# Kernel tuning notes

Hardware: AMD Instinct MI355X
Metric: run time of the kernel (lower is better)

The kernel has to match this reference:

```python
import jax, jax.numpy as jnp
import numpy as np

VOCAB = 100000
EMBED = 128
B = 65536
K = 10
EPS = 1e-10


def setup_inputs() -> dict:
    key = jax.random.key(0)
    k1, k2, k3, k4, k5 = jax.random.split(key, 5)
    init = 0.5 / EMBED
    t_weight = jax.random.uniform(k1, (VOCAB, EMBED), jnp.float32, -init, init)
    c_weight = jax.random.uniform(k2, (VOCAB, EMBED), jnp.float32, -init, init)
    t = jax.random.randint(k3, (B,), 0, VOCAB)
    c = jax.random.randint(k4, (B,), 0, VOCAB)
    n = jax.random.randint(k5, (B, K), 0, VOCAB)
    return {"t_weight": t_weight, "c_weight": c_weight, "t": t, "c": c, "n": n}


def reference(t_weight, c_weight, t, c, n):
    vt = t_weight[t]          # [B, D]
    vc = c_weight[c]          # [B, D]
    vn = c_weight[n]          # [B, K, D]
    pos_score = jnp.sum(vt * vc, axis=1)                     # [B]
    pos_loss = -jnp.mean(jnp.log(jax.nn.sigmoid(pos_score) + EPS))
    neg_score = jnp.einsum('bkd,bd->bk', vn, vt)             # [B, K]
    neg_loss = -jnp.mean(jnp.sum(jnp.log(jax.nn.sigmoid(-neg_score) + EPS), axis=1))
    return pos_loss + neg_loss
```

## Files before the change

kernel.cpp:

```cpp
#include <hip/hip_runtime.h>
#include <hip/hip_bf16.h>

constexpr int kEmbed = 128;
constexpr int kBatch = 65536;
constexpr int kNeg   = 10;
constexpr float kEps = 1e-10f;

__global__ __launch_bounds__(256, 4) void sgns_loss_kernel(
    const float* __restrict__ tw,
    const float* __restrict__ cw,
    const int*   __restrict__ t,
    const int*   __restrict__ c,
    const int*   __restrict__ n,
    float*       __restrict__ out)
{
    const int tid     = threadIdx.x;
    const int lane    = tid & 31;
    const int group   = (blockIdx.x * blockDim.x + tid) >> 5;
    const int ngroups = (gridDim.x * blockDim.x) >> 5;

    float acc = 0.0f;

    for (int b = group; b < kBatch; b += ngroups) {
        const int it = t[b];
        const int ic = c[b];
        int ni[kNeg];
        #pragma unroll
        for (int k = 0; k < kNeg; ++k) ni[k] = n[b * kNeg + k];

        const float4 vt = *reinterpret_cast<const float4*>(tw + (size_t)it * kEmbed + 4 * lane);
        const float4 vc = *reinterpret_cast<const float4*>(cw + (size_t)ic * kEmbed + 4 * lane);

        float s[kNeg + 1];
        s[0] = vt.x * vc.x + vt.y * vc.y + vt.z * vc.z + vt.w * vc.w;

        #pragma unroll
        for (int k = 0; k < kNeg; ++k) {
            const float4 vn = *reinterpret_cast<const float4*>(
                cw + (size_t)ni[k] * kEmbed + 4 * lane);
            s[k + 1] = vt.x * vn.x + vt.y * vn.y + vt.z * vn.z + vt.w * vn.w;
        }

        #pragma unroll
        for (int k = 0; k < kNeg + 1; ++k) {
            float v = s[k];
            v += __shfl_xor(v, 16);
            v += __shfl_xor(v, 8);
            v += __shfl_xor(v, 4);
            v += __shfl_xor(v, 2);
            v += __shfl_xor(v, 1);
            s[k] = v;
        }

        float lb = __logf(1.0f / (1.0f + __expf(-s[0])) + kEps);
        #pragma unroll
        for (int k = 1; k < kNeg + 1; ++k)
            lb += __logf(1.0f / (1.0f + __expf(s[k])) + kEps);

        if (lane == 0) acc += lb;
    }

    #pragma unroll
    for (int m = 32; m >= 1; m >>= 1) acc += __shfl_xor(acc, m);

    __shared__ float wave_sum[4];
    if ((tid & 63) == 0) wave_sum[tid >> 6] = acc;
    __syncthreads();
    if (tid == 0) {
        const float s4 = wave_sum[0] + wave_sum[1] + wave_sum[2] + wave_sum[3];
        atomicAdd(out, s4 * (-1.0f / (float)kBatch));
    }
}

extern "C" void kernel_launch(void* const* d_in, const int* in_sizes, int n_in,
                              void* d_out, int out_size, void* d_ws, size_t ws_size,
                              hipStream_t stream) {
    const float* tw = (const float*)d_in[0];
    const float* cw = (const float*)d_in[1];
    const int*   t  = (const int*)d_in[2];
    const int*   c  = (const int*)d_in[3];
    const int*   n  = (const int*)d_in[4];
    float* out = (float*)d_out;

    hipMemsetAsync(out, 0, sizeof(float), stream);

    sgns_loss_kernel<<<2048, 256, 0, stream>>>(tw, cw, t, c, n, out);
}
```

Measured before the change: 162.7 us.

## Map each sample to 8 threads with 64-byte loads, drop grid-stride loop

Each batch row is now handled by 8 lanes, each loading four float4 values (64 bytes) per embedding row, instead of 32 lanes each loading one float4. This cuts the shuffle reduction from five steps to three and puts more rows in flight per wave. The grid-stride loop is removed, so the fixed grid of 2048 blocks of 256 threads covers exactly 65536 rows. The cost is higher register pressure and a hard dependence on that launch geometry.

```diff
diff --git a/kernel.cpp b/kernel.cpp
--- a/kernel.cpp
+++ b/kernel.cpp
@@ -14,52 +14,56 @@
     const int*   __restrict__ n,
     float*       __restrict__ out)
 {
-    const int tid     = threadIdx.x;
-    const int lane    = tid & 31;
-    const int group   = (blockIdx.x * blockDim.x + tid) >> 5;
-    const int ngroups = (gridDim.x * blockDim.x) >> 5;
+    const int tid = threadIdx.x;
+    const int b   = (blockIdx.x * blockDim.x + tid) >> 3;
+    const int sub = tid & 7;
+    const int col = sub * 16;
 
-    float acc = 0.0f;
+    const int it = t[b];
+    const int ic = c[b];
+    int ni[kNeg];
+    #pragma unroll
+    for (int k = 0; k < kNeg; ++k) ni[k] = n[b * kNeg + k];
 
-    for (int b = group; b < kBatch; b += ngroups) {
-        const int it = t[b];
-        const int ic = c[b];
-        int ni[kNeg];
-        #pragma unroll
-        for (int k = 0; k < kNeg; ++k) ni[k] = n[b * kNeg + k];
+    const float4* vtp = reinterpret_cast<const float4*>(tw + (size_t)it * kEmbed + col);
+    const float4 vt0 = vtp[0], vt1 = vtp[1], vt2 = vtp[2], vt3 = vtp[3];
 
-        const float4 vt = *reinterpret_cast<const float4*>(tw + (size_t)it * kEmbed + 4 * lane);
-        const float4 vc = *reinterpret_cast<const float4*>(cw + (size_t)ic * kEmbed + 4 * lane);
+    float s[kNeg + 1];
 
-        float s[kNeg + 1];
-        s[0] = vt.x * vc.x + vt.y * vc.y + vt.z * vc.z + vt.w * vc.w;
-
-        #pragma unroll
-        for (int k = 0; k < kNeg; ++k) {
-            const float4 vn = *reinterpret_cast<const float4*>(
-                cw + (size_t)ni[k] * kEmbed + 4 * lane);
-            s[k + 1] = vt.x * vn.x + vt.y * vn.y + vt.z * vn.z + vt.w * vn.w;
-        }
-
-        #pragma unroll
-        for (int k = 0; k < kNeg + 1; ++k) {
-            float v = s[k];
-            v += __shfl_xor(v, 16);
-            v += __shfl_xor(v, 8);
-            v += __shfl_xor(v, 4);
-            v += __shfl_xor(v, 2);
-            v += __shfl_xor(v, 1);
-            s[k] = v;
-        }
-
-        float lb = __logf(1.0f / (1.0f + __expf(-s[0])) + kEps);
-        #pragma unroll
-        for (int k = 1; k < kNeg + 1; ++k)
-            lb += __logf(1.0f / (1.0f + __expf(s[k])) + kEps);
-
-        if (lane == 0) acc += lb;
+    {
+        const float4* vcp = reinterpret_cast<const float4*>(cw + (size_t)ic * kEmbed + col);
+        const float4 a = vcp[0], b4 = vcp[1], c4 = vcp[2], d4 = vcp[3];
+        s[0] = vt0.x*a.x + vt0.y*a.y + vt0.z*a.z + vt0.w*a.w
+             + vt1.x*b4.x + vt1.y*b4.y + vt1.z*b4.z + vt1.w*b4.w
+             + vt2.x*c4.x + vt2.y*c4.y + vt2.z*c4.z + vt2.w*c4.w
+             + vt3.x*d4.x + vt3.y*d4.y + vt3.z*d4.z + vt3.w*d4.w;
     }
 
+    #pragma unroll
+    for (int k = 0; k < kNeg; ++k) {
+        const float4* vnp = reinterpret_cast<const float4*>(cw + (size_t)ni[k] * kEmbed + col);
+        const float4 a = vnp[0], b4 = vnp[1], c4 = vnp[2], d4 = vnp[3];
+        s[k + 1] = vt0.x*a.x + vt0.y*a.y + vt0.z*a.z + vt0.w*a.w
+                 + vt1.x*b4.x + vt1.y*b4.y + vt1.z*b4.z + vt1.w*b4.w
+                 + vt2.x*c4.x + vt2.y*c4.y + vt2.z*c4.z + vt2.w*c4.w
+                 + vt3.x*d4.x + vt3.y*d4.y + vt3.z*d4.z + vt3.w*d4.w;
+    }
+
+    #pragma unroll
+    for (int k = 0; k < kNeg + 1; ++k) {
+        float v = s[k];
+        v += __shfl_xor(v, 4);
+        v += __shfl_xor(v, 2);
+        v += __shfl_xor(v, 1);
+        s[k] = v;
+    }
+
+    float lb = __logf(1.0f / (1.0f + __expf(-s[0])) + kEps);
+    #pragma unroll
+    for (int k = 1; k < kNeg + 1; ++k)
+        lb += __logf(1.0f / (1.0f + __expf(s[k])) + kEps);
+
+    float acc = (sub == 0) ? lb : 0.0f;
     #pragma unroll
     for (int m = 32; m >= 1; m >>= 1) acc += __shfl_xor(acc, m);
 
```

Result: slower. 232.1 us (+42.6%).
